# Kernel tuning notes

Hardware: AMD Instinct MI355X
Metric: run time of the kernel (lower is better)

## Reference

```python
import jax, jax.numpy as jnp
import numpy as np

IMAGE_W = 640
IMAGE_H = 640
ALPHA = 0.25
GAMMA = 2.0
BETA = 1.0 / 9.0
EPS = 1e-4


def _make_anchors(image_w, image_h):
    # standard RetinaNet anchors: 3 ratios x 3 scales per location, 5 FPN levels
    strides = [8, 16, 32, 64, 128]
    base_sizes = [32, 64, 128, 256, 512]
    ratios = np.array([0.5, 1.0, 2.0])
    scales = np.array([2.0 ** 0, 2.0 ** (1.0 / 3.0), 2.0 ** (2.0 / 3.0)])
    all_boxes = []
    for s, b in zip(strides, base_sizes):
        fw, fh = image_w // s, image_h // s
        ws, hs = [], []
        for r in ratios:
            for sc in scales:
                area = (b * sc) ** 2
                w = np.sqrt(area / r)
                ws.append(w)
                hs.append(w * r)
        wh = np.stack([np.array(ws), np.array(hs)], axis=-1).reshape(1, -1, 2)
        cx = (np.arange(fw) + 0.5) * s
        cy = (np.arange(fh) + 0.5) * s
        cx, cy = np.meshgrid(cx, cy)
        ctr = np.stack([cx, cy], axis=-1).reshape(-1, 1, 2)
        boxes = np.concatenate([ctr - 0.5 * wh, ctr + 0.5 * wh], axis=-1).reshape(-1, 4)
        all_boxes.append(boxes)
    return np.concatenate(all_boxes, axis=0).astype(np.float32)  # [76725, 4]


def setup_inputs() -> dict:
    key = jax.random.key(0)
    k1, k2, k3, k4, k5 = jax.random.split(key, 5)
    B, C, M = 4, 80, 16
    anchors = jnp.asarray(_make_anchors(IMAGE_W, IMAGE_H))  # [N,4]
    N = anchors.shape[0]
    batch_anchors = jnp.broadcast_to(anchors[None], (B, N, 4))
    cls_heads = jax.random.uniform(k1, (B, N, C), minval=0.01, maxval=0.99, dtype=jnp.float32)
    reg_heads = jax.random.normal(k2, (B, N, 4), dtype=jnp.float32)
    xy = jax.random.uniform(k3, (B, M, 2), minval=0.0, maxval=480.0)
    wh = jax.random.uniform(k4, (B, M, 2), minval=32.0, maxval=160.0)
    boxes = jnp.concatenate([xy, jnp.minimum(xy + wh, 639.0)], axis=-1)
    labels = jax.random.randint(k5, (B, M), 0, C).astype(jnp.float32)
    valid = jnp.arange(M)[None, :] < 12  # last 4 gt slots are -1 padding
    annotations = jnp.where(valid[..., None],
                            jnp.concatenate([boxes, labels[..., None]], axis=-1),
                            -1.0)
    return {"cls_heads": cls_heads, "reg_heads": reg_heads,
            "batch_anchors": batch_anchors, "annotations": annotations}


def _assign_one_image(anchors, annots):
    # anchors [N,4], annots [M,5] (label<0 == padding)
    valid_gt = annots[:, 4] >= 0.0                                  # [M]
    boxes, cls = annots[:, :4], annots[:, 4]
    area_a = (anchors[:, 2] - anchors[:, 0]) * (anchors[:, 3] - anchors[:, 1])
    area_g = (boxes[:, 2] - boxes[:, 0]) * (boxes[:, 3] - boxes[:, 1])
    lt = jnp.maximum(anchors[:, None, :2], boxes[None, :, :2])      # [N,M,2]
    rb = jnp.minimum(anchors[:, None, 2:], boxes[None, :, 2:])
    wh = jnp.clip(rb - lt, 0.0)
    inter = wh[..., 0] * wh[..., 1]                                 # [N,M]
    iou = inter / (area_a[:, None] + area_g[None, :] - inter)
    iou = jnp.where(valid_gt[None, :], iou, -1.0)                   # ignore padded gts
    idx = jnp.argmax(iou, axis=1)                                   # [N]
    overlap = jnp.max(iou, axis=1)
    gt_box = boxes[idx]                                             # [N,4]
    gt_cls = cls[idx]
    # encode gt box as (tx,ty,tw,th) wrt anchor
    a_wh = anchors[:, 2:] - anchors[:, :2]
    a_ctr = anchors[:, :2] + 0.5 * a_wh
    g_wh = jnp.clip(gt_box[:, 2:] - gt_box[:, :2], 1.0)
    g_ctr = gt_box[:, :2] + 0.5 * g_wh
    targets = jnp.concatenate([(g_ctr - a_ctr) / a_wh, jnp.log(g_wh / a_wh)], axis=1)
    targets = targets / jnp.array([0.1, 0.1, 0.2, 0.2], dtype=targets.dtype)
    label = jnp.full_like(overlap, -1.0)
    label = jnp.where(overlap < 0.4, 0.0, label)
    label = jnp.where(overlap > 0.5, gt_cls + 1.0, label)
    label = jnp.where(jnp.any(valid_gt), label, -1.0)               # no gt -> all ignore
    return targets, label


def reference(cls_heads, reg_heads, batch_anchors, annotations):
    # mask (instead of filter) out-of-border anchors: equivalent to dropping them
    a = batch_anchors
    inside = (a[..., 0] > 0) & (a[..., 1] > 0) & (a[..., 2] < IMAGE_W) & (a[..., 3] < IMAGE_H)
    targets, labels = jax.vmap(_assign_one_image)(batch_anchors, annotations)  # [B,N,4],[B,N]
    labels = jnp.where(inside, labels, -1.0)

    cls_mask = labels >= 0.0          # anchors counted in focal loss
    pos_mask = labels > 0.0           # positive anchors
    pos = jnp.sum(pos_mask, axis=1).astype(cls_heads.dtype)  # [B]

    # focal (cls) loss
    p = jnp.clip(cls_heads, EPS, 1.0 - EPS)                   # [B,N,C]
    num_classes = cls_heads.shape[-1]
    gt_onehot = jax.nn.one_hot(labels.astype(jnp.int32), num_classes + 1,
                               dtype=cls_heads.dtype)[..., 1:]  # [B,N,C]
    is_pos = gt_onehot > 0.5
    alpha_f = jnp.where(is_pos, ALPHA, 1.0 - ALPHA)
    pt = jnp.where(is_pos, p, 1.0 - p)
    focal_w = alpha_f * (1.0 - pt) ** GAMMA
    bce = -gt_onehot * jnp.log(p) - (1.0 - gt_onehot) * jnp.log(1.0 - p)
    fl = focal_w * bce
    cls_per_img = jnp.sum(fl * cls_mask[..., None], axis=(1, 2)) / jnp.maximum(pos, 1.0)

    # smooth-L1 (reg) loss over positive anchors
    x = jnp.abs(reg_heads - targets)
    sl1 = jnp.where(x < BETA, 0.5 * x * x / BETA, x - 0.5 * BETA)
    reg_per_img = jnp.sum(sl1 * pos_mask[..., None], axis=(1, 2)) / jnp.maximum(4.0 * pos, 1.0)

    valid_img = pos > 0.0
    n_valid = jnp.maximum(jnp.sum(valid_img.astype(cls_heads.dtype)), 1.0)
    cls_loss = jnp.sum(jnp.where(valid_img, cls_per_img, 0.0)) / n_valid
    reg_loss = jnp.sum(jnp.where(valid_img, reg_per_img, 0.0)) / n_valid
    return (cls_loss, reg_loss)
```

## Files before the change

kernel.cpp:

```cpp
#include <hip/hip_runtime.h>
#include <cmath>

#define GT_CAP 64
#define PF 4

typedef float fvec4 __attribute__((ext_vector_type(4)));

__global__ __launch_bounds__(256) void retina_main(
    const float* __restrict__ cls_heads,
    const float* __restrict__ reg_heads,
    const float* __restrict__ anchors,
    const float* __restrict__ annots,
    float* __restrict__ ws,
    int N, int M, int B)
{
    const int b  = blockIdx.y;
    const int n0 = blockIdx.x << 8;
    const int t  = threadIdx.x;

    __shared__ float s_ann[5 * GT_CAP];
    __shared__ float s_lab[256];
    __shared__ float s_red[12];

    const int mm = (M > GT_CAP) ? GT_CAP : M;
    for (int i = t; i < 5 * mm; i += 256)
        s_ann[i] = annots[(size_t)b * 5 * M + i];
    __syncthreads();

    float reg_acc = 0.0f;
    float pos_cnt = 0.0f;
    float label   = -1.0f;
    const int n = n0 + t;
    if (n < N) {
        const float4 a = *(const float4*)(anchors + (size_t)n * 4);
        const bool inside = (a.x > 0.0f) && (a.y > 0.0f) &&
                            (a.z < 640.0f) && (a.w < 640.0f);
        if (inside) {
            const float area_a = (a.z - a.x) * (a.w - a.y);
            float best = -3.0e38f;
            int   bi   = 0;
            bool  any  = false;
            for (int m = 0; m < mm; ++m) {
                const float gx1 = s_ann[m*5+0], gy1 = s_ann[m*5+1];
                const float gx2 = s_ann[m*5+2], gy2 = s_ann[m*5+3];
                const float gc  = s_ann[m*5+4];
                float v = -1.0f;
                if (gc >= 0.0f) {
                    any = true;
                    const float iw = fmaxf(fminf(a.z, gx2) - fmaxf(a.x, gx1), 0.0f);
                    const float ih = fmaxf(fminf(a.w, gy2) - fmaxf(a.y, gy1), 0.0f);
                    const float inter = iw * ih;
                    v = inter / (area_a + (gx2 - gx1) * (gy2 - gy1) - inter);
                }
                if (v > best) { best = v; bi = m; }
            }
            if (any) {
                if (best < 0.4f)      label = 0.0f;
                else if (best > 0.5f) label = s_ann[bi*5+4] + 1.0f;
            }
            if (label > 0.0f) {
                pos_cnt = 1.0f;
                const float aw = a.z - a.x, ah = a.w - a.y;
                const float acx = a.x + 0.5f * aw, acy = a.y + 0.5f * ah;
                const float gw = fmaxf(s_ann[bi*5+2] - s_ann[bi*5+0], 1.0f);
                const float gh = fmaxf(s_ann[bi*5+3] - s_ann[bi*5+1], 1.0f);
                const float gcx = s_ann[bi*5+0] + 0.5f * gw;
                const float gcy = s_ann[bi*5+1] + 0.5f * gh;
                const float tx = (gcx - acx) / aw * 10.0f;
                const float ty = (gcy - acy) / ah * 10.0f;
                const float tw = __logf(gw / aw) * 5.0f;
                const float th = __logf(gh / ah) * 5.0f;
                const float4 r = *(const float4*)(reg_heads + ((size_t)b * N + n) * 4);
                const float dx[4] = { fabsf(r.x - tx), fabsf(r.y - ty),
                                      fabsf(r.z - tw), fabsf(r.w - th) };
                #pragma unroll
                for (int j = 0; j < 4; ++j) {
                    const float x = dx[j];
                    reg_acc += (x < (1.0f / 9.0f)) ? 4.5f * x * x
                                                   : x - (1.0f / 18.0f);
                }
            }
        }
    }
    s_lab[t] = label;
    const int anyValid = __syncthreads_or(label >= 0.0f ? 1 : 0);

    float cls_acc = 0.0f;
    if (anyValid) {
        const float* cls_base = cls_heads + ((size_t)b * N + n0) * 80;
        int ap = t / 20, c4p = t - ap * 20;
        int c4c = c4p;
        float labb[PF];
        fvec4 pb[PF];
        #pragma unroll
        for (int k = 0; k < PF; ++k) {
            const float lab = s_lab[ap];
            fvec4 v = {0.5f, 0.5f, 0.5f, 0.5f};
            if (lab >= 0.0f) v = *(const fvec4*)(cls_base + 4 * t + 1024 * k);
            labb[k] = lab; pb[k] = v;
            ap += 12; c4p += 16; if (c4p >= 20) { c4p -= 20; ++ap; }
        }
        #pragma unroll
        for (int k = 0; k < 20; ++k) {
            const float lab = labb[k % PF];
            const fvec4 v   = pb[k % PF];
            if (k + PF < 20) {
                const float labn = s_lab[ap];
                fvec4 vn = {0.5f, 0.5f, 0.5f, 0.5f};
                if (labn >= 0.0f)
                    vn = *(const fvec4*)(cls_base + 4 * t + 1024 * (k + PF));
                labb[k % PF] = labn; pb[k % PF] = vn;
                ap += 12; c4p += 16; if (c4p >= 20) { c4p -= 20; ++ap; }
            }
            const float mask = (lab >= 0.0f) ? 1.0f : 0.0f;
            const float pv[4] = { v.x, v.y, v.z, v.w };
            const float cb = (float)(c4c * 4 + 1);
            float local = 0.0f;
            #pragma unroll
            for (int j = 0; j < 4; ++j) {
                const float p = fminf(fmaxf(pv[j], 1.0e-4f), 1.0f - 1.0e-4f);
                const bool  is_pos = (lab == cb + (float)j);
                const float pt     = is_pos ? p : 1.0f - p;
                const float alpha  = is_pos ? 0.25f : 0.75f;
                const float om     = 1.0f - pt;
                local += alpha * om * om * (-__logf(pt));
            }
            cls_acc += mask * local;
            c4c += 16; if (c4c >= 20) c4c -= 20;
        }
    }

    const int lane = t & 63, wid = t >> 6;
    #pragma unroll
    for (int off = 32; off > 0; off >>= 1) {
        cls_acc += __shfl_down(cls_acc, off, 64);
        reg_acc += __shfl_down(reg_acc, off, 64);
        pos_cnt += __shfl_down(pos_cnt, off, 64);
    }
    if (lane == 0) {
        s_red[wid]     = cls_acc;
        s_red[4 + wid] = reg_acc;
        s_red[8 + wid] = pos_cnt;
    }
    __syncthreads();
    if (t == 0) {
        const float c = s_red[0] + s_red[1] + s_red[2]  + s_red[3];
        const float r = s_red[4] + s_red[5] + s_red[6]  + s_red[7];
        const float p = s_red[8] + s_red[9] + s_red[10] + s_red[11];
        if (c != 0.0f) atomicAdd(&ws[b], c);
        if (r != 0.0f) atomicAdd(&ws[B + b], r);
        if (p != 0.0f) atomicAdd(&ws[2 * B + b], p);
    }
}

__global__ void retina_final(const float* __restrict__ ws,
                             float* __restrict__ out, int B)
{
    if (threadIdx.x == 0 && blockIdx.x == 0) {
        float cl = 0.0f, rl = 0.0f, nv = 0.0f;
        for (int b = 0; b < B; ++b) {
            const float pos = ws[2 * B + b];
            if (pos > 0.0f) {
                cl += ws[b]     / fmaxf(pos, 1.0f);
                rl += ws[B + b] / fmaxf(4.0f * pos, 1.0f);
                nv += 1.0f;
            }
        }
        const float n = fmaxf(nv, 1.0f);
        out[0] = cl / n;
        out[1] = rl / n;
    }
}

extern "C" void kernel_launch(void* const* d_in, const int* in_sizes, int n_in,
                              void* d_out, int out_size, void* d_ws, size_t ws_size,
                              hipStream_t stream) {
    const float* cls = (const float*)d_in[0];
    const float* reg = (const float*)d_in[1];
    const float* anc = (const float*)d_in[2];
    const float* ann = (const float*)d_in[3];

    const int B = 4;
    const int N = in_sizes[1] / (4 * B);
    const int M = in_sizes[3] / (5 * B);
    float* ws = (float*)d_ws;

    (void)hipMemsetAsync(d_ws, 0, 12 * sizeof(float), stream);

    dim3 grid((N + 255) / 256, B);
    retina_main<<<grid, 256, 0, stream>>>(cls, reg, anc, ann, ws, N, M, B);
    retina_final<<<1, 64, 0, stream>>>(ws, (float*)d_out, B);
}
```

Baseline: 164.6 us.

## Shrink per-block anchor tile to 64 and issue all cls loads upfront

```diff
diff --git a/kernel.cpp b/kernel.cpp
--- a/kernel.cpp
+++ b/kernel.cpp
@@ -2,7 +2,6 @@
 #include <cmath>
 
 #define GT_CAP 64
-#define PF 4
 
 typedef float fvec4 __attribute__((ext_vector_type(4)));
 
@@ -15,11 +14,11 @@
     int N, int M, int B)
 {
     const int b  = blockIdx.y;
-    const int n0 = blockIdx.x << 8;
+    const int n0 = blockIdx.x << 6;
     const int t  = threadIdx.x;
 
     __shared__ float s_ann[5 * GT_CAP];
-    __shared__ float s_lab[256];
+    __shared__ float s_lab[64];
     __shared__ float s_red[12];
 
     const int mm = (M > GT_CAP) ? GT_CAP : M;
@@ -30,91 +29,87 @@
     float reg_acc = 0.0f;
     float pos_cnt = 0.0f;
     float label   = -1.0f;
-    const int n = n0 + t;
-    if (n < N) {
-        const float4 a = *(const float4*)(anchors + (size_t)n * 4);
-        const bool inside = (a.x > 0.0f) && (a.y > 0.0f) &&
-                            (a.z < 640.0f) && (a.w < 640.0f);
-        if (inside) {
-            const float area_a = (a.z - a.x) * (a.w - a.y);
-            float best = -3.0e38f;
-            int   bi   = 0;
-            bool  any  = false;
-            for (int m = 0; m < mm; ++m) {
-                const float gx1 = s_ann[m*5+0], gy1 = s_ann[m*5+1];
-                const float gx2 = s_ann[m*5+2], gy2 = s_ann[m*5+3];
-                const float gc  = s_ann[m*5+4];
-                float v = -1.0f;
-                if (gc >= 0.0f) {
-                    any = true;
-                    const float iw = fmaxf(fminf(a.z, gx2) - fmaxf(a.x, gx1), 0.0f);
-                    const float ih = fmaxf(fminf(a.w, gy2) - fmaxf(a.y, gy1), 0.0f);
-                    const float inter = iw * ih;
-                    v = inter / (area_a + (gx2 - gx1) * (gy2 - gy1) - inter);
+    if (t < 64) {
+        const int n = n0 + t;
+        if (n < N) {
+            const float4 a = *(const float4*)(anchors + (size_t)n * 4);
+            const bool inside = (a.x > 0.0f) && (a.y > 0.0f) &&
+                                (a.z < 640.0f) && (a.w < 640.0f);
+            if (inside) {
+                const float area_a = (a.z - a.x) * (a.w - a.y);
+                float best = -3.0e38f;
+                int   bi   = 0;
+                bool  any  = false;
+                for (int m = 0; m < mm; ++m) {
+                    const float gx1 = s_ann[m*5+0], gy1 = s_ann[m*5+1];
+                    const float gx2 = s_ann[m*5+2], gy2 = s_ann[m*5+3];
+                    const float gc  = s_ann[m*5+4];
+                    float v = -1.0f;
+                    if (gc >= 0.0f) {
+                        any = true;
+                        const float iw = fmaxf(fminf(a.z, gx2) - fmaxf(a.x, gx1), 0.0f);
+                        const float ih = fmaxf(fminf(a.w, gy2) - fmaxf(a.y, gy1), 0.0f);
+                        const float inter = iw * ih;
+                        v = inter / (area_a + (gx2 - gx1) * (gy2 - gy1) - inter);
+                    }
+                    if (v > best) { best = v; bi = m; }
                 }
-                if (v > best) { best = v; bi = m; }
-            }
-            if (any) {
-                if (best < 0.4f)      label = 0.0f;
-                else if (best > 0.5f) label = s_ann[bi*5+4] + 1.0f;
-            }
-            if (label > 0.0f) {
-                pos_cnt = 1.0f;
-                const float aw = a.z - a.x, ah = a.w - a.y;
-                const float acx = a.x + 0.5f * aw, acy = a.y + 0.5f * ah;
-                const float gw = fmaxf(s_ann[bi*5+2] - s_ann[bi*5+0], 1.0f);
-                const float gh = fmaxf(s_ann[bi*5+3] - s_ann[bi*5+1], 1.0f);
-                const float gcx = s_ann[bi*5+0] + 0.5f * gw;
-                const float gcy = s_ann[bi*5+1] + 0.5f * gh;
-                const float tx = (gcx - acx) / aw * 10.0f;
-                const float ty = (gcy - acy) / ah * 10.0f;
-                const float tw = __logf(gw / aw) * 5.0f;
-                const float th = __logf(gh / ah) * 5.0f;
-                const float4 r = *(const float4*)(reg_heads + ((size_t)b * N + n) * 4);
-                const float dx[4] = { fabsf(r.x - tx), fabsf(r.y - ty),
-                                      fabsf(r.z - tw), fabsf(r.w - th) };
-                #pragma unroll
-                for (int j = 0; j < 4; ++j) {
-                    const float x = dx[j];
-                    reg_acc += (x < (1.0f / 9.0f)) ? 4.5f * x * x
-                                                   : x - (1.0f / 18.0f);
+                if (any) {
+                    if (best < 0.4f)      label = 0.0f;
+                    else if (best > 0.5f) label = s_ann[bi*5+4] + 1.0f;
+                }
+                if (label > 0.0f) {
+                    pos_cnt = 1.0f;
+                    const float aw = a.z - a.x, ah = a.w - a.y;
+                    const float acx = a.x + 0.5f * aw, acy = a.y + 0.5f * ah;
+                    const float gw = fmaxf(s_ann[bi*5+2] - s_ann[bi*5+0], 1.0f);
+                    const float gh = fmaxf(s_ann[bi*5+3] - s_ann[bi*5+1], 1.0f);
+                    const float gcx = s_ann[bi*5+0] + 0.5f * gw;
+                    const float gcy = s_ann[bi*5+1] + 0.5f * gh;
+                    const float tx = (gcx - acx) / aw * 10.0f;
+                    const float ty = (gcy - acy) / ah * 10.0f;
+                    const float tw = __logf(gw / aw) * 5.0f;
+                    const float th = __logf(gh / ah) * 5.0f;
+                    const float4 r = *(const float4*)(reg_heads + ((size_t)b * N + n) * 4);
+                    const float dx[4] = { fabsf(r.x - tx), fabsf(r.y - ty),
+                                          fabsf(r.z - tw), fabsf(r.w - th) };
+                    #pragma unroll
+                    for (int j = 0; j < 4; ++j) {
+                        const float x = dx[j];
+                        reg_acc += (x < (1.0f / 9.0f)) ? 4.5f * x * x
+                                                       : x - (1.0f / 18.0f);
+                    }
                 }
             }
         }
+        s_lab[t] = label;
     }
-    s_lab[t] = label;
-    const int anyValid = __syncthreads_or(label >= 0.0f ? 1 : 0);
+    const int anyValid = __syncthreads_or((t < 64 && label >= 0.0f) ? 1 : 0);
 
     float cls_acc = 0.0f;
     if (anyValid) {
         const float* cls_base = cls_heads + ((size_t)b * N + n0) * 80;
-        int ap = t / 20, c4p = t - ap * 20;
-        int c4c = c4p;
-        float labb[PF];
-        fvec4 pb[PF];
+        float labb[5];
+        fvec4 pb[5];
         #pragma unroll
-        for (int k = 0; k < PF; ++k) {
-            const float lab = s_lab[ap];
+        for (int k = 0; k < 5; ++k) {
+            const int e = t + (k << 8);
+            const int a = e / 20;
+            const float lab = s_lab[a];
             fvec4 v = {0.5f, 0.5f, 0.5f, 0.5f};
-            if (lab >= 0.0f) v = *(const fvec4*)(cls_base + 4 * t + 1024 * k);
+            if (lab >= 0.0f)
+                v = *(const fvec4*)(cls_base + 4 * e);
             labb[k] = lab; pb[k] = v;
-            ap += 12; c4p += 16; if (c4p >= 20) { c4p -= 20; ++ap; }
         }
         #pragma unroll
-        for (int k = 0; k < 20; ++k) {
-            const float lab = labb[k % PF];
-            const fvec4 v   = pb[k % PF];
-            if (k + PF < 20) {
-                const float labn = s_lab[ap];
-                fvec4 vn = {0.5f, 0.5f, 0.5f, 0.5f};
-                if (labn >= 0.0f)
-                    vn = *(const fvec4*)(cls_base + 4 * t + 1024 * (k + PF));
-                labb[k % PF] = labn; pb[k % PF] = vn;
-                ap += 12; c4p += 16; if (c4p >= 20) { c4p -= 20; ++ap; }
-            }
+        for (int k = 0; k < 5; ++k) {
+            const int e  = t + (k << 8);
+            const int c4 = e - (e / 20) * 20;
+            const float lab  = labb[k];
+            const fvec4 v    = pb[k];
             const float mask = (lab >= 0.0f) ? 1.0f : 0.0f;
             const float pv[4] = { v.x, v.y, v.z, v.w };
-            const float cb = (float)(c4c * 4 + 1);
+            const float cb = (float)(c4 * 4 + 1);
             float local = 0.0f;
             #pragma unroll
             for (int j = 0; j < 4; ++j) {
@@ -126,7 +121,6 @@
                 local += alpha * om * om * (-__logf(pt));
             }
             cls_acc += mask * local;
-            c4c += 16; if (c4c >= 20) c4c -= 20;
         }
     }
 
@@ -187,7 +181,7 @@
 
     (void)hipMemsetAsync(d_ws, 0, 12 * sizeof(float), stream);
 
-    dim3 grid((N + 255) / 256, B);
+    dim3 grid((N + 63) / 64, B);
     retina_main<<<grid, 256, 0, stream>>>(cls, reg, anc, ann, ws, N, M, B);
     retina_final<<<1, 64, 0, stream>>>(ws, (float*)d_out, B);
 }
```

Result: slower. 199.2 us (+21.0%).
